# Kernel tuning notes

Hardware: AMD Instinct MI355X
Metric: run time of the kernel (lower is better)

The kernel has to match this reference:

```python
import jax, jax.numpy as jnp
import numpy as np

B, T, N_STOCKS = 256, 250, 500
HIDDEN, N_LAYERS = 512, 2
LB, UB = 0.0, 0.1
N_ITER = 30  # rebalance fixed-point iterations; extra iters are exact no-ops once converged


def setup_inputs() -> dict:
    key = jax.random.key(0)
    ks = jax.random.split(key, 16)
    s = 1.0 / np.sqrt(HIDDEN)  # torch GRU init scale
    inp = {"x": jax.random.normal(ks[0], (B, T, N_STOCKS), jnp.float32)}
    in_dims = [N_STOCKS, HIDDEN]
    for l in range(N_LAYERS):
        inp[f"w_ih_l{l}"] = jax.random.uniform(ks[1 + 4 * l], (3 * HIDDEN, in_dims[l]), jnp.float32, -s, s)
        inp[f"w_hh_l{l}"] = jax.random.uniform(ks[2 + 4 * l], (3 * HIDDEN, HIDDEN), jnp.float32, -s, s)
        inp[f"b_ih_l{l}"] = jax.random.uniform(ks[3 + 4 * l], (3 * HIDDEN,), jnp.float32, -s, s)
        inp[f"b_hh_l{l}"] = jax.random.uniform(ks[4 + 4 * l], (3 * HIDDEN,), jnp.float32, -s, s)
    inp["fc_w"] = jax.random.uniform(ks[9], (N_STOCKS, HIDDEN), jnp.float32, -s, s)
    inp["fc_b"] = jax.random.uniform(ks[10], (N_STOCKS,), jnp.float32, -s, s)
    return inp


def gru_layer(x, w_ih, w_hh, b_ih, b_hh):
    # x: [B, T, D] -> hidden sequence [B, T, H]; torch gate order: r, z, n
    gi = jnp.einsum('btd,gd->btg', x, w_ih) + b_ih  # precompute input gates [B, T, 3H]

    def cell(h, gi_t):
        gh = h @ w_hh.T + b_hh
        i_r, i_z, i_n = jnp.split(gi_t, 3, axis=-1)
        h_r, h_z, h_n = jnp.split(gh, 3, axis=-1)
        r = jax.nn.sigmoid(i_r + h_r)
        z = jax.nn.sigmoid(i_z + h_z)
        n = jnp.tanh(i_n + r * h_n)
        h_new = (1.0 - z) * n + z * h
        return h_new, h_new

    h0 = jnp.zeros((x.shape[0], HIDDEN), x.dtype)
    _, hs = jax.lax.scan(cell, h0, jnp.swapaxes(gi, 0, 1))  # scan over time
    return jnp.swapaxes(hs, 0, 1)


def rebalance(w):
    # Batched capped-simplex redistribution: clamp to [LB, UB], then push the
    # clipped mass onto non-capped entries proportionally; repeat to fixed point.
    def body(w, _):
        wc = jnp.clip(w, LB, UB)
        leftover = jnp.sum(w - wc, axis=-1, keepdims=True)
        nom = jnp.where(wc != UB, wc, 0.0)
        w_new = wc + leftover * nom / jnp.sum(nom, axis=-1, keepdims=True)
        return w_new, None

    w, _ = jax.lax.scan(body, w, None, length=N_ITER)
    return w


def reference(x, w_ih_l0, w_hh_l0, b_ih_l0, b_hh_l0,
              w_ih_l1, w_hh_l1, b_ih_l1, b_hh_l1, fc_w, fc_b):
    h = gru_layer(x, w_ih_l0, w_hh_l0, b_ih_l0, b_hh_l0)
    h = gru_layer(h, w_ih_l1, w_hh_l1, b_ih_l1, b_hh_l1)
    h_t = h[:, -1, :]                      # last timestep [B, H]
    logit = h_t @ fc_w.T + fc_b            # dropout is identity at inference
    logit = jax.nn.silu(logit)             # swish
    w = jax.nn.softmax(logit, axis=-1)
    return rebalance(w)
```

## Files before the change

kernel.cpp:

```cpp
#include <hip/hip_runtime.h>
#include <math.h>

typedef __attribute__((ext_vector_type(8))) short short8;
typedef __attribute__((ext_vector_type(4))) float floatx4;
typedef unsigned short ushort_t;
typedef unsigned int uint32;
typedef unsigned long long u64;

#define BB 256
#define TT 250
#define NS 500
#define HH 512
#define NBLK 256
#define TBLK 512
#define PL_USH 131072u
#define CH_USH 8192u
#define WHI_USH 32768
#define SMEMB 131072

__device__ __forceinline__ ushort_t f2bf(float f) {
    uint32 u = __float_as_uint(f);
    u += 0x7fffu + ((u >> 16) & 1u);
    return (ushort_t)(u >> 16);
}
__device__ __forceinline__ float bf2f(ushort_t h) { return __uint_as_float(((uint32)h) << 16); }
__device__ __forceinline__ float sigm(float x) { return 1.f / (1.f + expf(-x)); }
__device__ __forceinline__ floatx4 mfma16(short8 a, short8 b, floatx4 c) {
    return __builtin_amdgcn_mfma_f32_16x16x32_bf16(a, b, c, 0, 0, 0);
}
__device__ __forceinline__ u64 pack4(const ushort_t* a) {
    return (u64)a[0] | ((u64)a[1] << 16) | ((u64)a[2] << 32) | ((u64)a[3] << 48);
}
__device__ __forceinline__ void st_agent_u64(ushort_t* p, u64 v) {
    __hip_atomic_store((u64*)p, v, __ATOMIC_RELAXED, __HIP_MEMORY_SCOPE_AGENT);
}
__device__ __forceinline__ void st_agent_u64x(uint4* p, uint4 v) {
    u64* q = (u64*)p;
    __hip_atomic_store(q,     (u64)v.x | ((u64)v.y << 32), __ATOMIC_RELAXED, __HIP_MEMORY_SCOPE_AGENT);
    __hip_atomic_store(q + 1, (u64)v.z | ((u64)v.w << 32), __ATOMIC_RELAXED, __HIP_MEMORY_SCOPE_AGENT);
}

__device__ __forceinline__ void dbar(unsigned* flags, unsigned phase, int bid) {
    __syncthreads();
    if (threadIdx.x == 0)
        __hip_atomic_store(flags + ((size_t)bid << 4), phase,
                           __ATOMIC_RELAXED, __HIP_MEMORY_SCOPE_AGENT);
    if (threadIdx.x < NBLK) {
        unsigned* sp = flags + ((size_t)threadIdx.x << 4);
        while (__hip_atomic_load(sp, __ATOMIC_RELAXED, __HIP_MEMORY_SCOPE_AGENT) < phase)
            __builtin_amdgcn_s_sleep(2);
    }
    __syncthreads();
}

__device__ __forceinline__ float block_max8(float v, float* scr) {
#pragma unroll
    for (int off = 32; off; off >>= 1) v = fmaxf(v, __shfl_down(v, off, 64));
    if ((threadIdx.x & 63) == 0) scr[threadIdx.x >> 6] = v;
    __syncthreads();
    if (threadIdx.x == 0) {
        float m = scr[0];
#pragma unroll
        for (int w = 1; w < 8; ++w) m = fmaxf(m, scr[w]);
        scr[16] = m;
    }
    __syncthreads();
    float r = scr[16];
    __syncthreads();
    return r;
}
__device__ __forceinline__ float2 block_sum2_8(float a, float b, float* scr) {
#pragma unroll
    for (int off = 32; off; off >>= 1) {
        a += __shfl_down(a, off, 64);
        b += __shfl_down(b, off, 64);
    }
    if ((threadIdx.x & 63) == 0) { int w = threadIdx.x >> 6; scr[w] = a; scr[8 + w] = b; }
    __syncthreads();
    if (threadIdx.x == 0) {
        float sa = 0.f, sb = 0.f;
#pragma unroll
        for (int w = 0; w < 8; ++w) { sa += scr[w]; sb += scr[8 + w]; }
        scr[16] = sa; scr[17] = sb;
    }
    __syncthreads();
    float2 r = make_float2(scr[16], scr[17]);
    __syncthreads();
    return r;
}

__device__ __forceinline__ void gemm_both(const ushort_t* __restrict__ gp,
                                          const ushort_t* __restrict__ hp,
                                          const ushort_t* whiS, const ushort_t* wloS,
                                          floatx4 (&aGI)[2], floatx4 (&aGH)[2]) {
    short8 Bh[12], Bl[12];
    const ushort_t* gpl = gp + PL_USH;
    const ushort_t* hpl = hp + PL_USH;

#define ISSUE(pc) do {                                                                    \
        const ushort_t* _ph = ((pc) < 16) ? (gp + (size_t)(pc) * CH_USH)                  \
                                          : (hp + (size_t)((pc) - 16) * CH_USH);          \
        const ushort_t* _pl = ((pc) < 16) ? (gpl + (size_t)(pc) * CH_USH)                 \
                                          : (hpl + (size_t)((pc) - 16) * CH_USH);         \
        asm volatile("global_load_dwordx4 %0, %1, off sc0 sc1"                            \
                     : "=v"(Bh[(pc) % 12]) : "v"(_ph));                                   \
        asm volatile("global_load_dwordx4 %0, %1, off sc0 sc1"                            \
                     : "=v"(Bl[(pc) % 12]) : "v"(_pl));                                   \
    } while (0)

    ISSUE(0); ISSUE(1); ISSUE(2); ISSUE(3); ISSUE(4); ISSUE(5);
    ISSUE(6); ISSUE(7); ISSUE(8); ISSUE(9); ISSUE(10);

    short8 w0h = *(const short8*)(whiS);
    short8 w1h = *(const short8*)(whiS + 512);
    short8 w0l = *(const short8*)(wloS);
    short8 w1l = *(const short8*)(wloS + 512);

#define GSTEP(c, N) do {                                                                  \
        if ((c) + 11 < 32) ISSUE((c) + 11);                                               \
        short8 n0h, n1h, n0l, n1l;                                                        \
        if ((c) + 1 < 32) {                                                               \
            const size_t _w = (size_t)(((c) + 1) * 2) * 512;                              \
            n0h = *(const short8*)(whiS + _w);                                            \
            n1h = *(const short8*)(whiS + _w + 512);                                      \
            n0l = *(const short8*)(wloS + _w);                                            \
            n1l = *(const short8*)(wloS + _w + 512);                                      \
        }                                                                                 \
        asm volatile("s_waitcnt vmcnt(" #N ")" ::: "memory");                             \
        __builtin_amdgcn_sched_barrier(0);                                                \
        const int _cs = (c) % 12;                                                         \
        floatx4 (&A)[2] = ((c) < 16) ? aGI : aGH;                                         \
        A[0] = mfma16(w0h, Bh[_cs], A[0]);                                                \
        A[1] = mfma16(w1h, Bh[_cs], A[1]);                                                \
        A[0] = mfma16(w0h, Bl[_cs], A[0]);                                                \
        A[1] = mfma16(w1h, Bl[_cs], A[1]);                                                \
        A[0] = mfma16(w0l, Bh[_cs], A[0]);                                                \
        A[1] = mfma16(w1l, Bh[_cs], A[1]);                                                \
        if ((c) + 1 < 32) { w0h = n0h; w1h = n1h; w0l = n0l; w1l = n1l; }                 \
    } while (0)

    GSTEP(0, 22);  GSTEP(1, 22);  GSTEP(2, 22);  GSTEP(3, 22);  GSTEP(4, 22);
    GSTEP(5, 22);  GSTEP(6, 22);  GSTEP(7, 22);  GSTEP(8, 22);  GSTEP(9, 22);
    GSTEP(10, 22); GSTEP(11, 22); GSTEP(12, 22); GSTEP(13, 22); GSTEP(14, 22);
    GSTEP(15, 22); GSTEP(16, 22); GSTEP(17, 22); GSTEP(18, 22); GSTEP(19, 22);
    GSTEP(20, 22); GSTEP(21, 20); GSTEP(22, 18); GSTEP(23, 16); GSTEP(24, 14);
    GSTEP(25, 12); GSTEP(26, 10); GSTEP(27, 8);  GSTEP(28, 6);  GSTEP(29, 4);
    GSTEP(30, 2);  GSTEP(31, 0);
#undef GSTEP
#undef ISSUE
}

__global__ void __launch_bounds__(TBLK, 2)
gru_main(const float* __restrict__ x,
         const float* __restrict__ wih0, const float* __restrict__ whh0,
         const float* __restrict__ bi0,  const float* __restrict__ bh0,
         const float* __restrict__ wih1, const float* __restrict__ whh1,
         const float* __restrict__ bi1,  const float* __restrict__ bh1,
         const float* __restrict__ fcb,  const float* __restrict__ fcT,
         ushort_t* xpack, ushort_t* h0pack, ushort_t* h1pack,
         unsigned* flags,
         float* __restrict__ out)
{
    extern __shared__ char smem_raw[];
    ushort_t* whi = (ushort_t*)smem_raw;
    ushort_t* wlo = whi + WHI_USH;

    const int bid = blockIdx.x, tid = threadIdx.x;
    const int L  = bid >> 7;
    const int UG = (bid >> 1) & 63;
    const int CT = bid & 1;
    const int wid = tid >> 6, lane = tid & 63;

    {
        const float* Wgi = L ? wih1 : wih0;
        const float* Wgh = L ? whh1 : whh0;
        const int Kgi = L ? HH : NS;
        for (int idx = tid; idx < 32768; idx += TBLK) {
            const int j = idx & 7, ln = (idx >> 3) & 63, rc = idx >> 9;
            const int c = rc >> 1, rt = rc & 1;
            const int m = ln & 15, qq = ln >> 4;
            const int lr = rt * 16 + m;
            const int g = lr >> 3, u = lr & 7;
            float v = 0.f;
            if (g < 3) {
                if (c < 16) {
                    const int k = c * 32 + qq * 8 + j;
                    if (k < Kgi) v = Wgi[(size_t)(g * HH + UG * 8 + u) * Kgi + k];
                } else {
                    const int k = (c - 16) * 32 + qq * 8 + j;
                    v = Wgh[(size_t)(g * HH + UG * 8 + u) * HH + k];
                }
            }
            const ushort_t hb = f2bf(v);
            whi[idx] = hb;
            wlo[idx] = f2bf(v - bf2f(hb));
        }
    }

    const int ub = ((lane >> 4) & 1) * 4;
    float biR[4], biZ[4], biN[4], bhR[4], bhZ[4], bhN[4];
    {
        const float* bi = L ? bi1 : bi0;
        const float* bh = L ? bh1 : bh0;
#pragma unroll
        for (int p = 0; p < 4; ++p) {
            const int ugl = UG * 8 + ub + p;
            biR[p] = bi[ugl]; biZ[p] = bi[HH + ugl]; biN[p] = bi[2 * HH + ugl];
            bhR[p] = bh[ugl]; bhZ[p] = bh[HH + ugl]; bhN[p] = bh[2 * HH + ugl];
        }
    }
    float hreg[4] = {0.f, 0.f, 0.f, 0.f};
    const int chW = UG >> 2, qqW = UG & 3;
    __syncthreads();

    const ushort_t* whiS = whi + (size_t)lane * 8;
    const ushort_t* wloS = wlo + (size_t)lane * 8;
    const size_t apoff = ((size_t)(CT * 8 + wid) * 64 + lane) * 8;

    for (int s = 0; s <= TT; ++s) {
        const unsigned phase = (unsigned)s + 1;
        const bool active = L ? (s >= 1) : (s < TT);
        if (active) {
            const ushort_t *gisrc, *ghsrc;
            if (L == 0) {
                gisrc = xpack + (size_t)(s & 1) * 2 * PL_USH;
                ghsrc = h0pack + (size_t)((s - 1) & 1) * 2 * PL_USH;
            } else {
                gisrc = h0pack + (size_t)((s - 1) & 1) * 2 * PL_USH;
                ghsrc = h1pack + (size_t)(s & 1) * 2 * PL_USH;
            }
            floatx4 z4 = {0.f, 0.f, 0.f, 0.f};
            floatx4 aGI[2], aGH[2];
            aGI[0] = z4; aGI[1] = z4; aGH[0] = z4; aGH[1] = z4;
            gemm_both(gisrc + apoff, ghsrc + apoff, whiS, wloS, aGI, aGH);

            float4 xv0, xv1;
            const bool doX = (s <= TT - 2) && (bid * TBLK + tid < 16384);
            int xko = 0, xb = 0;
            if (doX) {
                const int gx = bid * TBLK + tid;
                xko = gx & 63; xb = gx >> 6;
                const float* xs = x + ((size_t)xb * TT + (s + 1)) * NS + xko * 8;
                if (xko < 62) { xv0 = *(const float4*)(xs); xv1 = *(const float4*)(xs + 4); }
                else {
                    float tmp[8];
#pragma unroll
                    for (int j = 0; j < 8; ++j) {
                        const int k = xko * 8 + j;
                        tmp[j] = (k < NS) ? xs[j] : 0.f;
                    }
                    xv0 = make_float4(tmp[0], tmp[1], tmp[2], tmp[3]);
                    xv1 = make_float4(tmp[4], tmp[5], tmp[6], tmp[7]);
                }
            }

            float zGI[4], zGH[4];
#pragma unroll
            for (int r = 0; r < 4; ++r) {
                zGI[r] = __shfl_xor(aGI[0][r], 32, 64);
                zGH[r] = __shfl_xor(aGH[0][r], 32, 64);
            }
            ushort_t* pk = L ? h1pack + (size_t)((s - 1) & 1) * 2 * PL_USH
                             : h0pack + (size_t)(s & 1) * 2 * PL_USH;
            if (lane < 32) {
                ushort_t hi4[4], lo4[4];
#pragma unroll
                for (int r = 0; r < 4; ++r) {
                    const float gir = aGI[0][r], ghr = aGH[0][r];
                    const float giz = zGI[r],    ghz = zGH[r];
                    const float gin = aGI[1][r], ghn = aGH[1][r];
                    const float rr = sigm(gir + biR[r] + ghr + bhR[r]);
                    const float zz = sigm(giz + biZ[r] + ghz + bhZ[r]);
                    const float nn = tanhf(gin + biN[r] + rr * (ghn + bhN[r]));
                    const float hv = (1.f - zz) * nn + zz * hreg[r];
                    hreg[r] = hv;
                    hi4[r] = f2bf(hv);
                    lo4[r] = f2bf(hv - bf2f(hi4[r]));
                }
                const int b = CT * 128 + wid * 16 + (lane & 15);
                const size_t o8 = ((size_t)(chW * 16 + (b >> 4)) * 64 + qqW * 16 + (b & 15)) * 8 + ub;
                st_agent_u64(pk + o8, pack4(hi4));
                st_agent_u64(pk + PL_USH + o8, pack4(lo4));
            }

            if (doX) {
                ushort_t hi8[8], lo8[8];
                float vv[8] = {xv0.x, xv0.y, xv0.z, xv0.w, xv1.x, xv1.y, xv1.z, xv1.w};
#pragma unroll
                for (int j = 0; j < 8; ++j) {
                    hi8[j] = f2bf(vv[j]);
                    lo8[j] = f2bf(vv[j] - bf2f(hi8[j]));
                }
                ushort_t* xp = xpack + (size_t)((s + 1) & 1) * 2 * PL_USH;
                const size_t o = ((size_t)((xko >> 2) * 16 + (xb >> 4)) * 64 + (xko & 3) * 16 + (xb & 15)) * 8;
                st_agent_u64(xp + o, pack4(hi8));
                st_agent_u64(xp + o + 4, pack4(hi8 + 4));
                st_agent_u64(xp + PL_USH + o, pack4(lo8));
                st_agent_u64(xp + PL_USH + o + 4, pack4(lo8 + 4));
            }
        } else if ((s <= TT - 2) && (bid * TBLK + tid < 16384)) {
            const int gx = bid * TBLK + tid;
            const int xko = gx & 63, xb = gx >> 6;
            const float* xs = x + ((size_t)xb * TT + (s + 1)) * NS + xko * 8;
            ushort_t hi8[8], lo8[8];
#pragma unroll
            for (int j = 0; j < 8; ++j) {
                const int k = xko * 8 + j;
                const float v = (k < NS) ? xs[j] : 0.f;
                hi8[j] = f2bf(v);
                lo8[j] = f2bf(v - bf2f(hi8[j]));
            }
            ushort_t* xp = xpack + (size_t)((s + 1) & 1) * 2 * PL_USH;
            const size_t o = ((size_t)((xko >> 2) * 16 + (xb >> 4)) * 64 + (xko & 3) * 16 + (xb & 15)) * 8;
            st_agent_u64(xp + o, pack4(hi8));
            st_agent_u64(xp + o + 4, pack4(hi8 + 4));
            st_agent_u64(xp + PL_USH + o, pack4(lo8));
            st_agent_u64(xp + PL_USH + o + 4, pack4(lo8 + 4));
        }
        dbar(flags, phase, bid);
    }

    {
        const int b = bid;
        float* sh = (float*)smem_raw;
        float* scr = sh + 512;
        const ushort_t* pk = h1pack + (size_t)1 * 2 * PL_USH;
        {
            const int u = tid;
            const int uo = u >> 3, j = u & 7;
            const size_t o = ((size_t)((uo >> 2) * 16 + (b >> 4)) * 64 + (uo & 3) * 16 + (b & 15)) * 8 + j;
            sh[u] = bf2f(pk[o]) + bf2f(pk[PL_USH + o]);
        }
        __syncthreads();

        const bool valid = tid < NS;
        const int o1 = valid ? tid : 0;
        float a0 = fcb[o1];
        for (int k = 0; k < HH; ++k)
            a0 = fmaf(sh[k], fcT[(size_t)k * NS + o1], a0);
        float l0 = a0 * sigm(a0);
        float mx = block_max8(valid ? l0 : -3.4e38f, scr);
        float e0 = valid ? expf(l0 - mx) : 0.f;
        float2 s2 = block_sum2_8(e0, 0.f, scr);
        float w0 = e0 / s2.x;
        for (int it = 0; it < 30; ++it) {
            float c0v = fminf(fmaxf(w0, 0.f), 0.1f);
            float lv = w0 - c0v;
            float n0 = (c0v != 0.1f) ? c0v : 0.f;
            float2 rs = block_sum2_8(lv, n0, scr);
            w0 = c0v + rs.x / rs.y * n0;
        }
        if (valid) out[(size_t)b * NS + tid] = w0;
    }
}

__global__ void pack_x0(const float* __restrict__ x, ushort_t* __restrict__ xpack) {
    const int t = blockIdx.x * 256 + threadIdx.x;
    const int ko = t & 63, b = t >> 6;
    const float* xs = x + (size_t)b * TT * NS;
    ushort_t hi8[8], lo8[8];
#pragma unroll
    for (int j = 0; j < 8; ++j) {
        const int k = ko * 8 + j;
        const float v = (k < NS) ? xs[k] : 0.f;
        hi8[j] = f2bf(v);
        lo8[j] = f2bf(v - bf2f(hi8[j]));
    }
    const size_t o = ((size_t)((ko >> 2) * 16 + (b >> 4)) * 64 + (ko & 3) * 16 + (b & 15)) * 8;
    *(uint4*)(xpack + o) = *(uint4*)hi8;
    *(uint4*)(xpack + PL_USH + o) = *(uint4*)lo8;
}

__global__ void transpose_k(const float* __restrict__ src, float* __restrict__ dst,
                            int G, int K) {
    int idx = blockIdx.x * 256 + threadIdx.x;
    if (idx >= G * K) return;
    int k = idx / G, g = idx - k * G;
    dst[idx] = src[(size_t)g * K + k];
}

extern "C" void kernel_launch(void* const* d_in, const int* in_sizes, int n_in,
                              void* d_out, int out_size, void* d_ws, size_t ws_size,
                              hipStream_t stream) {
    const float* x    = (const float*)d_in[0];
    const float* wih0 = (const float*)d_in[1];
    const float* whh0 = (const float*)d_in[2];
    const float* bih0 = (const float*)d_in[3];
    const float* bhh0 = (const float*)d_in[4];
    const float* wih1 = (const float*)d_in[5];
    const float* whh1 = (const float*)d_in[6];
    const float* bih1 = (const float*)d_in[7];
    const float* bhh1 = (const float*)d_in[8];
    const float* fcw  = (const float*)d_in[9];
    const float* fcb  = (const float*)d_in[10];
    float* outp = (float*)d_out;

    char* ws = (char*)d_ws;
    unsigned* flags  = (unsigned*)ws;
    ushort_t* h0pack = (ushort_t*)(ws + 196608);
    ushort_t* h1pack = (ushort_t*)(ws + 196608 + 1048576);
    ushort_t* xpack  = (ushort_t*)(ws + 196608 + 2097152);
    float*    fcT    = (float*)(ws + 196608 + 3145728);

    hipMemsetAsync(ws, 0, 196608 + 2097152, stream);
    pack_x0<<<64, 256, 0, stream>>>(x, xpack);
    {
        int nel = NS * HH;
        transpose_k<<<(nel + 255) / 256, 256, 0, stream>>>(fcw, fcT, NS, HH);
    }

    hipFuncSetAttribute((const void*)gru_main,
                        hipFuncAttributeMaxDynamicSharedMemorySize, SMEMB);

    void* args[] = {(void*)&x,
                    (void*)&wih0, (void*)&whh0, (void*)&bih0, (void*)&bhh0,
                    (void*)&wih1, (void*)&whh1, (void*)&bih1, (void*)&bhh1,
                    (void*)&fcb, (void*)&fcT,
                    (void*)&xpack, (void*)&h0pack, (void*)&h1pack,
                    (void*)&flags, (void*)&outp};
    hipError_t e = hipLaunchCooperativeKernel((const void*)gru_main, dim3(NBLK), dim3(TBLK),
                                              args, SMEMB, stream);
    if (e != hipSuccess) {
        gru_main<<<dim3(NBLK), dim3(TBLK), SMEMB, stream>>>(
            x, wih0, whh0, bih0, bhh0, wih1, whh1, bih1, bhh1,
            fcb, fcT, xpack, h0pack, h1pack, flags, outp);
    }
}
```

Baseline: 3.327 ms.

## Split GRU work into four pipelined roles with input-gate partials via global buffer

Adds a new persistent kernel where the 256 blocks are split into four roles (layer0 input GEMM, layer0 hidden GEMM, layer1 input GEMM, layer1 hidden GEMM). Each role handles 32 unit groups with 3 gate tiles. The input-gate roles write partial gate sums to a global P buffer, and the hidden roles consume them one step later, forming a 4-stage pipeline over 253 steps. This halves the per-block GEMM K-depth on the critical path and shrinks shared memory. In exchange it adds global round-trips for the partials, an extra waitcnt before each grid barrier, and a workspace-size-dependent fallback to the old kernel.

```diff
diff --git a/kernel.cpp b/kernel.cpp
--- a/kernel.cpp
+++ b/kernel.cpp
@@ -15,8 +15,18 @@
 #define TBLK 512
 #define PL_USH 131072u
 #define CH_USH 8192u
+#define WP_USH 24576
+#define SMEMB_SPLIT (WP_USH * 2 * 2)
+#define PPAR 393216
+#define NSTEP 253
 #define WHI_USH 32768
-#define SMEMB 131072
+#define SMEMB_U8 131072
+
+#define WS_FLAGS   196608
+#define WS_PACKS   (3 * 1048576)
+#define WS_FCT     1024000
+#define WS_PBUF    (4 * PPAR * 4)
+#define WS_NEED_SPLIT ((size_t)(WS_FLAGS + WS_PACKS + WS_FCT + WS_PBUF))
 
 __device__ __forceinline__ ushort_t f2bf(float f) {
     uint32 u = __float_as_uint(f);
@@ -34,13 +44,15 @@
 __device__ __forceinline__ void st_agent_u64(ushort_t* p, u64 v) {
     __hip_atomic_store((u64*)p, v, __ATOMIC_RELAXED, __HIP_MEMORY_SCOPE_AGENT);
 }
-__device__ __forceinline__ void st_agent_u64x(uint4* p, uint4 v) {
+__device__ __forceinline__ void st_agent_f4(float* p, floatx4 v) {
+    union { floatx4 f; u64 q[2]; } cv; cv.f = v;
     u64* q = (u64*)p;
-    __hip_atomic_store(q,     (u64)v.x | ((u64)v.y << 32), __ATOMIC_RELAXED, __HIP_MEMORY_SCOPE_AGENT);
-    __hip_atomic_store(q + 1, (u64)v.z | ((u64)v.w << 32), __ATOMIC_RELAXED, __HIP_MEMORY_SCOPE_AGENT);
+    __hip_atomic_store(q,     cv.q[0], __ATOMIC_RELAXED, __HIP_MEMORY_SCOPE_AGENT);
+    __hip_atomic_store(q + 1, cv.q[1], __ATOMIC_RELAXED, __HIP_MEMORY_SCOPE_AGENT);
 }
 
 __device__ __forceinline__ void dbar(unsigned* flags, unsigned phase, int bid) {
+    asm volatile("s_waitcnt vmcnt(0)" ::: "memory");
     __syncthreads();
     if (threadIdx.x == 0)
         __hip_atomic_store(flags + ((size_t)bid << 4), phase,
@@ -87,6 +99,65 @@
     float2 r = make_float2(scr[16], scr[17]);
     __syncthreads();
     return r;
+}
+
+__device__ __forceinline__ void gemm_one(const ushort_t* __restrict__ gp,
+                                         const ushort_t* whiS, const ushort_t* wloS,
+                                         floatx4 (&acc)[3]) {
+    short8 Bh[12], Bl[12];
+
+#define ISSUE1(pc) do {                                                                   \
+        const ushort_t* _p = gp + (size_t)(pc) * CH_USH;                                  \
+        asm volatile("global_load_dwordx4 %0, %1, off sc0 sc1"                            \
+                     : "=v"(Bh[(pc) % 12]) : "v"(_p));                                    \
+        asm volatile("global_load_dwordx4 %0, %1, off sc0 sc1"                            \
+                     : "=v"(Bl[(pc) % 12]) : "v"(_p + PL_USH));                           \
+    } while (0)
+
+    ISSUE1(0); ISSUE1(1); ISSUE1(2); ISSUE1(3); ISSUE1(4); ISSUE1(5);
+    ISSUE1(6); ISSUE1(7); ISSUE1(8); ISSUE1(9); ISSUE1(10); ISSUE1(11);
+
+    short8 w0h = *(const short8*)(whiS);
+    short8 w1h = *(const short8*)(whiS + 512);
+    short8 w2h = *(const short8*)(whiS + 1024);
+    short8 w0l = *(const short8*)(wloS);
+    short8 w1l = *(const short8*)(wloS + 512);
+    short8 w2l = *(const short8*)(wloS + 1024);
+
+#define GSTEP1(c, N) do {                                                                 \
+        short8 n0h, n1h, n2h, n0l, n1l, n2l;                                              \
+        if ((c) + 1 < 16) {                                                               \
+            const size_t _w = (size_t)((c) + 1) * 3 * 512;                                \
+            n0h = *(const short8*)(whiS + _w);                                            \
+            n1h = *(const short8*)(whiS + _w + 512);                                      \
+            n2h = *(const short8*)(whiS + _w + 1024);                                     \
+            n0l = *(const short8*)(wloS + _w);                                            \
+            n1l = *(const short8*)(wloS + _w + 512);                                      \
+            n2l = *(const short8*)(wloS + _w + 1024);                                     \
+        }                                                                                 \
+        asm volatile("s_waitcnt vmcnt(" #N ")" ::: "memory");                             \
+        __builtin_amdgcn_sched_barrier(0);                                                \
+        const int _cs = (c) % 12;                                                         \
+        acc[0] = mfma16(w0h, Bh[_cs], acc[0]);                                            \
+        acc[1] = mfma16(w1h, Bh[_cs], acc[1]);                                            \
+        acc[2] = mfma16(w2h, Bh[_cs], acc[2]);                                            \
+        acc[0] = mfma16(w0h, Bl[_cs], acc[0]);                                            \
+        acc[1] = mfma16(w1h, Bl[_cs], acc[1]);                                            \
+        acc[2] = mfma16(w2h, Bl[_cs], acc[2]);                                            \
+        acc[0] = mfma16(w0l, Bh[_cs], acc[0]);                                            \
+        acc[1] = mfma16(w1l, Bh[_cs], acc[1]);                                            \
+        acc[2] = mfma16(w2l, Bh[_cs], acc[2]);                                            \
+        if ((c) + 12 < 16) ISSUE1((c) + 12);                                              \
+        if ((c) + 1 < 16) { w0h = n0h; w1h = n1h; w2h = n2h;                              \
+                            w0l = n0l; w1l = n1l; w2l = n2l; }                            \
+    } while (0)
+
+    GSTEP1(0, 22);  GSTEP1(1, 22);  GSTEP1(2, 22);  GSTEP1(3, 22);  GSTEP1(4, 22);
+    GSTEP1(5, 20);  GSTEP1(6, 18);  GSTEP1(7, 16);  GSTEP1(8, 14);  GSTEP1(9, 12);
+    GSTEP1(10, 10); GSTEP1(11, 8);  GSTEP1(12, 6);  GSTEP1(13, 4);  GSTEP1(14, 2);
+    GSTEP1(15, 0);
+#undef GSTEP1
+#undef ISSUE1
 }
 
 __device__ __forceinline__ void gemm_both(const ushort_t* __restrict__ gp,
@@ -150,16 +221,205 @@
 #undef ISSUE
 }
 
+__device__ __forceinline__ void epilogue(char* smem_raw, int bid, int tid,
+                                         const ushort_t* h1pack,
+                                         const float* fcb, const float* fcT,
+                                         float* out) {
+    const int b = bid;
+    float* sh = (float*)smem_raw;
+    float* scr = sh + 512;
+    const ushort_t* pk = h1pack + (size_t)1 * 2 * PL_USH;
+    {
+        const int u = tid;
+        const int uo = u >> 3, j = u & 7;
+        const size_t o = ((size_t)((uo >> 2) * 16 + (b >> 4)) * 64 + (uo & 3) * 16 + (b & 15)) * 8 + j;
+        sh[u] = bf2f(pk[o]) + bf2f(pk[PL_USH + o]);
+    }
+    __syncthreads();
+
+    const bool valid = tid < NS;
+    const int o1 = valid ? tid : 0;
+    float a0 = fcb[o1];
+    for (int k = 0; k < HH; ++k)
+        a0 = fmaf(sh[k], fcT[(size_t)k * NS + o1], a0);
+    float l0 = a0 * sigm(a0);
+    float mx = block_max8(valid ? l0 : -3.4e38f, scr);
+    float e0 = valid ? expf(l0 - mx) : 0.f;
+    float2 s2 = block_sum2_8(e0, 0.f, scr);
+    float w0 = e0 / s2.x;
+    for (int it = 0; it < 30; ++it) {
+        float c0v = fminf(fmaxf(w0, 0.f), 0.1f);
+        float lv = w0 - c0v;
+        float n0 = (c0v != 0.1f) ? c0v : 0.f;
+        float2 rs = block_sum2_8(lv, n0, scr);
+        w0 = c0v + rs.x / rs.y * n0;
+    }
+    if (valid) out[(size_t)b * NS + tid] = w0;
+}
+
 __global__ void __launch_bounds__(TBLK, 2)
-gru_main(const float* __restrict__ x,
-         const float* __restrict__ wih0, const float* __restrict__ whh0,
-         const float* __restrict__ bi0,  const float* __restrict__ bh0,
-         const float* __restrict__ wih1, const float* __restrict__ whh1,
-         const float* __restrict__ bi1,  const float* __restrict__ bh1,
-         const float* __restrict__ fcb,  const float* __restrict__ fcT,
-         ushort_t* xpack, ushort_t* h0pack, ushort_t* h1pack,
-         unsigned* flags,
-         float* __restrict__ out)
+gru_split(const float* __restrict__ x,
+          const float* __restrict__ wih0, const float* __restrict__ whh0,
+          const float* __restrict__ bi0,  const float* __restrict__ bh0,
+          const float* __restrict__ wih1, const float* __restrict__ whh1,
+          const float* __restrict__ bi1,  const float* __restrict__ bh1,
+          const float* __restrict__ fcb,  const float* __restrict__ fcT,
+          ushort_t* xpack, ushort_t* h0pack, ushort_t* h1pack,
+          float* Pbuf, unsigned* flags,
+          float* __restrict__ out)
+{
+    extern __shared__ char smem_raw[];
+    ushort_t* whi = (ushort_t*)smem_raw;
+    ushort_t* wlo = whi + WP_USH;
+
+    const int bid = blockIdx.x, tid = threadIdx.x;
+    const int role = bid >> 6;
+    const int UG = (bid >> 1) & 31;
+    const int CT = bid & 1;
+    const int wid = tid >> 6, lane = tid & 63;
+    const bool isGH = role & 1;
+
+    {
+        const float* Wsrc = (role == 0) ? wih0 : (role == 1) ? whh0
+                           : (role == 2) ? wih1 : whh1;
+        const int Ksrc = (role == 0) ? NS : HH;
+        for (int idx = tid; idx < WP_USH; idx += TBLK) {
+            const int j = idx & 7, ln = (idx >> 3) & 63, rc = idx >> 9;
+            const int c = rc / 3, rt = rc - c * 3;
+            const int m = ln & 15, qq = ln >> 4;
+            const int k = c * 32 + qq * 8 + j;
+            float v = 0.f;
+            if (k < Ksrc) v = Wsrc[(size_t)(rt * HH + UG * 16 + m) * Ksrc + k];
+            const ushort_t hb = f2bf(v);
+            whi[idx] = hb;
+            wlo[idx] = f2bf(v - bf2f(hb));
+        }
+    }
+
+    float biR[4], biZ[4], biN[4], bhR[4], bhZ[4], bhN[4];
+    if (isGH) {
+        const float* bi = (role == 1) ? bi0 : bi1;
+        const float* bh = (role == 1) ? bh0 : bh1;
+#pragma unroll
+        for (int r = 0; r < 4; ++r) {
+            const int ugl = UG * 16 + ((lane >> 4) * 4 + r);
+            biR[r] = bi[ugl]; biZ[r] = bi[HH + ugl]; biN[r] = bi[2 * HH + ugl];
+            bhR[r] = bh[ugl]; bhZ[r] = bh[HH + ugl]; bhN[r] = bh[2 * HH + ugl];
+        }
+    }
+    float hreg[4] = {0.f, 0.f, 0.f, 0.f};
+    __syncthreads();
+
+    const ushort_t* whiS = whi + (size_t)lane * 8;
+    const ushort_t* wloS = wlo + (size_t)lane * 8;
+    const size_t apoff = ((size_t)(CT * 8 + wid) * 64 + lane) * 8;
+    float* Pmy = Pbuf + (size_t)(role >> 1) * (2 * PPAR)
+               + (((size_t)(UG * 2 + CT) * 8 + wid) * 3) * 256 + (size_t)lane * 4;
+
+    for (int s = 0; s < NSTEP; ++s) {
+        bool active;
+        switch (role) {
+            case 0:  active = (s <= 249); break;
+            case 1:  active = (s >= 1 && s <= 250); break;
+            case 2:  active = (s >= 2 && s <= 251); break;
+            default: active = (s >= 3 && s <= 252); break;
+        }
+        if (active) {
+            const ushort_t* srcb = (role == 0) ? xpack : (role == 3) ? h1pack : h0pack;
+            const ushort_t* src = srcb + (size_t)(s & 1) * 2 * PL_USH + apoff;
+
+            floatx4 pr, pz, pn;
+            if (isGH) {
+                const float* Pr = Pmy + (size_t)((s - 1) & 1) * PPAR;
+                asm volatile("global_load_dwordx4 %0, %1, off sc0 sc1" : "=v"(pr) : "v"(Pr));
+                asm volatile("global_load_dwordx4 %0, %1, off sc0 sc1" : "=v"(pz) : "v"(Pr + 256));
+                asm volatile("global_load_dwordx4 %0, %1, off sc0 sc1" : "=v"(pn) : "v"(Pr + 512));
+            }
+
+            floatx4 z4 = {0.f, 0.f, 0.f, 0.f};
+            floatx4 acc[3] = {z4, z4, z4};
+            gemm_one(src, whiS, wloS, acc);
+
+            float4 xv0, xv1;
+            const bool doX = (s <= TT - 2) && (bid * TBLK + tid < 16384);
+            int xko = 0, xb = 0;
+            if (doX) {
+                const int gx = bid * TBLK + tid;
+                xko = gx & 63; xb = gx >> 6;
+                const float* xs = x + ((size_t)xb * TT + (s + 1)) * NS + xko * 8;
+                if (xko < 62) { xv0 = *(const float4*)(xs); xv1 = *(const float4*)(xs + 4); }
+                else {
+                    float tmp[8];
+#pragma unroll
+                    for (int j = 0; j < 8; ++j) {
+                        const int k = xko * 8 + j;
+                        tmp[j] = (k < NS) ? xs[j] : 0.f;
+                    }
+                    xv0 = make_float4(tmp[0], tmp[1], tmp[2], tmp[3]);
+                    xv1 = make_float4(tmp[4], tmp[5], tmp[6], tmp[7]);
+                }
+            }
+
+            if (!isGH) {
+                float* Pw = Pmy + (size_t)(s & 1) * PPAR;
+                st_agent_f4(Pw,       acc[0]);
+                st_agent_f4(Pw + 256, acc[1]);
+                st_agent_f4(Pw + 512, acc[2]);
+            } else {
+                ushort_t hi4[4], lo4[4];
+#pragma unroll
+                for (int r = 0; r < 4; ++r) {
+                    const float rr = sigm(pr[r] + biR[r] + acc[0][r] + bhR[r]);
+                    const float zz = sigm(pz[r] + biZ[r] + acc[1][r] + bhZ[r]);
+                    const float nn = tanhf(pn[r] + biN[r] + rr * (acc[2][r] + bhN[r]));
+                    const float hv = (1.f - zz) * nn + zz * hreg[r];
+                    hreg[r] = hv;
+                    hi4[r] = f2bf(hv);
+                    lo4[r] = f2bf(hv - bf2f(hi4[r]));
+                }
+                ushort_t* pk = ((role == 1) ? h0pack : h1pack)
+                             + (size_t)((s - 1) & 1) * 2 * PL_USH;
+                const int u0 = UG * 16 + (lane >> 4) * 4;
+                const int uo = u0 >> 3, j0 = u0 & 7;
+                const int b = CT * 128 + wid * 16 + (lane & 15);
+                const size_t o8 = ((size_t)((uo >> 2) * 16 + (b >> 4)) * 64
+                                  + (uo & 3) * 16 + (b & 15)) * 8 + j0;
+                st_agent_u64(pk + o8, pack4(hi4));
+                st_agent_u64(pk + PL_USH + o8, pack4(lo4));
+            }
+
+            if (doX) {
+                ushort_t hi8[8], lo8[8];
+                float vv[8] = {xv0.x, xv0.y, xv0.z, xv0.w, xv1.x, xv1.y, xv1.z, xv1.w};
+#pragma unroll
+                for (int j = 0; j < 8; ++j) {
+                    hi8[j] = f2bf(vv[j]);
+                    lo8[j] = f2bf(vv[j] - bf2f(hi8[j]));
+                }
+                ushort_t* xp = xpack + (size_t)((s + 1) & 1) * 2 * PL_USH;
+                const size_t o = ((size_t)((xko >> 2) * 16 + (xb >> 4)) * 64 + (xko & 3) * 16 + (xb & 15)) * 8;
+                st_agent_u64(xp + o, pack4(hi8));
+                st_agent_u64(xp + o + 4, pack4(hi8 + 4));
+                st_agent_u64(xp + PL_USH + o, pack4(lo8));
+                st_agent_u64(xp + PL_USH + o + 4, pack4(lo8 + 4));
+            }
+        }
+        dbar(flags, (unsigned)s + 1, bid);
+    }
+
+    epilogue(smem_raw, bid, tid, h1pack, fcb, fcT, out);
+}
+
+__global__ void __launch_bounds__(TBLK, 2)
+gru_u8(const float* __restrict__ x,
+       const float* __restrict__ wih0, const float* __restrict__ whh0,
+       const float* __restrict__ bi0,  const float* __restrict__ bh0,
+       const float* __restrict__ wih1, const float* __restrict__ whh1,
+       const float* __restrict__ bi1,  const float* __restrict__ bh1,
+       const float* __restrict__ fcb,  const float* __restrict__ fcT,
+       ushort_t* xpack, ushort_t* h0pack, ushort_t* h1pack,
+       float* Pbuf, unsigned* flags,
+       float* __restrict__ out)
 {
     extern __shared__ char smem_raw[];
     ushort_t* whi = (ushort_t*)smem_raw;
@@ -298,60 +558,11 @@
                 st_agent_u64(xp + PL_USH + o, pack4(lo8));
                 st_agent_u64(xp + PL_USH + o + 4, pack4(lo8 + 4));
             }
-        } else if ((s <= TT - 2) && (bid * TBLK + tid < 16384)) {
-            const int gx = bid * TBLK + tid;
-            const int xko = gx & 63, xb = gx >> 6;
-            const float* xs = x + ((size_t)xb * TT + (s + 1)) * NS + xko * 8;
-            ushort_t hi8[8], lo8[8];
-#pragma unroll
-            for (int j = 0; j < 8; ++j) {
-                const int k = xko * 8 + j;
-                const float v = (k < NS) ? xs[j] : 0.f;
-                hi8[j] = f2bf(v);
-                lo8[j] = f2bf(v - bf2f(hi8[j]));
-            }
-            ushort_t* xp = xpack + (size_t)((s + 1) & 1) * 2 * PL_USH;
-            const size_t o = ((size_t)((xko >> 2) * 16 + (xb >> 4)) * 64 + (xko & 3) * 16 + (xb & 15)) * 8;
-            st_agent_u64(xp + o, pack4(hi8));
-            st_agent_u64(xp + o + 4, pack4(hi8 + 4));
-            st_agent_u64(xp + PL_USH + o, pack4(lo8));
-            st_agent_u64(xp + PL_USH + o + 4, pack4(lo8 + 4));
         }
         dbar(flags, phase, bid);
     }
 
-    {
-        const int b = bid;
-        float* sh = (float*)smem_raw;
-        float* scr = sh + 512;
-        const ushort_t* pk = h1pack + (size_t)1 * 2 * PL_USH;
-        {
-            const int u = tid;
-            const int uo = u >> 3, j = u & 7;
-            const size_t o = ((size_t)((uo >> 2) * 16 + (b >> 4)) * 64 + (uo & 3) * 16 + (b & 15)) * 8 + j;
-            sh[u] = bf2f(pk[o]) + bf2f(pk[PL_USH + o]);
-        }
-        __syncthreads();
-
-        const bool valid = tid < NS;
-        const int o1 = valid ? tid : 0;
-        float a0 = fcb[o1];
-        for (int k = 0; k < HH; ++k)
-            a0 = fmaf(sh[k], fcT[(size_t)k * NS + o1], a0);
-        float l0 = a0 * sigm(a0);
-        float mx = block_max8(valid ? l0 : -3.4e38f, scr);
-        float e0 = valid ? expf(l0 - mx) : 0.f;
-        float2 s2 = block_sum2_8(e0, 0.f, scr);
-        float w0 = e0 / s2.x;
-        for (int it = 0; it < 30; ++it) {
-            float c0v = fminf(fmaxf(w0, 0.f), 0.1f);
-            float lv = w0 - c0v;
-            float n0 = (c0v != 0.1f) ? c0v : 0.f;
-            float2 rs = block_sum2_8(lv, n0, scr);
-            w0 = c0v + rs.x / rs.y * n0;
-        }
-        if (valid) out[(size_t)b * NS + tid] = w0;
-    }
+    epilogue(smem_raw, bid, tid, h1pack, fcb, fcT, out);
 }
 
 __global__ void pack_x0(const float* __restrict__ x, ushort_t* __restrict__ xpack) {
@@ -397,32 +608,47 @@
 
     char* ws = (char*)d_ws;
     unsigned* flags  = (unsigned*)ws;
-    ushort_t* h0pack = (ushort_t*)(ws + 196608);
-    ushort_t* h1pack = (ushort_t*)(ws + 196608 + 1048576);
-    ushort_t* xpack  = (ushort_t*)(ws + 196608 + 2097152);
-    float*    fcT    = (float*)(ws + 196608 + 3145728);
-
-    hipMemsetAsync(ws, 0, 196608 + 2097152, stream);
+    ushort_t* h0pack = (ushort_t*)(ws + WS_FLAGS);
+    ushort_t* h1pack = (ushort_t*)(ws + WS_FLAGS + 1048576);
+    ushort_t* xpack  = (ushort_t*)(ws + WS_FLAGS + 2097152);
+    float*    fcT    = (float*)(ws + WS_FLAGS + 3145728);
+    float*    Pbuf   = (float*)(ws + WS_FLAGS + 3145728 + WS_FCT);
+
+    const bool useSplit = (ws_size == 0) || (ws_size >= WS_NEED_SPLIT);
+
+    hipMemsetAsync(ws, 0, WS_FLAGS + 2097152, stream);
     pack_x0<<<64, 256, 0, stream>>>(x, xpack);
     {
         int nel = NS * HH;
         transpose_k<<<(nel + 255) / 256, 256, 0, stream>>>(fcw, fcT, NS, HH);
     }
 
-    hipFuncSetAttribute((const void*)gru_main,
-                        hipFuncAttributeMaxDynamicSharedMemorySize, SMEMB);
+    hipFuncSetAttribute((const void*)gru_split,
+                        hipFuncAttributeMaxDynamicSharedMemorySize, SMEMB_SPLIT);
+    hipFuncSetAttribute((const void*)gru_u8,
+                        hipFuncAttributeMaxDynamicSharedMemorySize, SMEMB_U8);
 
     void* args[] = {(void*)&x,
                     (void*)&wih0, (void*)&whh0, (void*)&bih0, (void*)&bhh0,
                     (void*)&wih1, (void*)&whh1, (void*)&bih1, (void*)&bhh1,
                     (void*)&fcb, (void*)&fcT,
                     (void*)&xpack, (void*)&h0pack, (void*)&h1pack,
-                    (void*)&flags, (void*)&outp};
-    hipError_t e = hipLaunchCooperativeKernel((const void*)gru_main, dim3(NBLK), dim3(TBLK),
-                                              args, SMEMB, stream);
-    if (e != hipSuccess) {
-        gru_main<<<dim3(NBLK), dim3(TBLK), SMEMB, stream>>>(
-            x, wih0, whh0, bih0, bhh0, wih1, whh1, bih1, bhh1,
-            fcb, fcT, xpack, h0pack, h1pack, flags, outp);
-    }
-}
+                    (void*)&Pbuf, (void*)&flags, (void*)&outp};
+    if (useSplit) {
+        hipError_t e = hipLaunchCooperativeKernel((const void*)gru_split, dim3(NBLK), dim3(TBLK),
+                                                  args, SMEMB_SPLIT, stream);
+        if (e != hipSuccess) {
+            gru_split<<<dim3(NBLK), dim3(TBLK), SMEMB_SPLIT, stream>>>(
+                x, wih0, whh0, bih0, bhh0, wih1, whh1, bih1, bhh1,
+                fcb, fcT, xpack, h0pack, h1pack, Pbuf, flags, outp);
+        }
+    } else {
+        hipError_t e = hipLaunchCooperativeKernel((const void*)gru_u8, dim3(NBLK), dim3(TBLK),
+                                                  args, SMEMB_U8, stream);
+        if (e != hipSuccess) {
+            gru_u8<<<dim3(NBLK), dim3(TBLK), SMEMB_U8, stream>>>(
+                x, wih0, whh0, bih0, bhh0, wih1, whh1, bih1, bhh1,
+                fcb, fcT, xpack, h0pack, h1pack, Pbuf, flags, outp);
+        }
+    }
+}
```

After: 3.136 ms. -5.7%, faster.
